# Kernel tuning notes

Hardware: AMD Instinct MI355X
Metric: run time of the kernel (lower is better)

The kernel has to match this reference:

```python
import jax, jax.numpy as jnp
import numpy as np
from jax import lax

B, T, D, H, L = 16, 1500, 512, 512, 2
LN_EPS = 1e-5


def _layernorm(v, w, b):
    m = jnp.mean(v, axis=-1, keepdims=True)
    var = jnp.mean(jnp.square(v - m), axis=-1, keepdims=True)
    return (v - m) * lax.rsqrt(var + LN_EPS) * w + b


def setup_inputs() -> dict:
    key = jax.random.key(0)
    k_x, k_wi, k_wh = jax.random.split(key, 3)
    x = jax.random.normal(k_x, (B, T, D), dtype=jnp.float32)
    # i2h / h2h weights: [L, 3H, in_dim] (input_size == hidden_size so stackable)
    Wi = jax.random.normal(k_wi, (L, 3 * H, D), dtype=jnp.float32) * 0.04
    Wh = jax.random.normal(k_wh, (L, 3 * H, H), dtype=jnp.float32) * 0.04
    # LayerNorm affine params for (r, z, n) per layer
    ln_w = jnp.ones((L, 3, H), dtype=jnp.float32)
    ln_b = jnp.zeros((L, 3, H), dtype=jnp.float32)
    return {"x": x, "Wi": Wi, "Wh": Wh, "ln_w": ln_w, "ln_b": ln_b}


def reference(x, Wi, Wh, ln_w, ln_b):
    n_layers = Wi.shape[0]
    hidden = Wh.shape[-1]
    batch = x.shape[0]

    def step(h_states, x_t):
        # h_states: [L, B, H]; x_t: [B, D]
        inp = x_t
        new_hs = []
        for l in range(n_layers):
            h = h_states[l]
            x_gates = inp @ Wi[l].T        # [B, 3H]
            h_gates = h @ Wh[l].T          # [B, 3H]
            x_r, x_z, x_n = jnp.split(x_gates, 3, axis=1)
            h_r, h_z, h_n = jnp.split(h_gates, 3, axis=1)
            r = jax.nn.sigmoid(_layernorm(x_r + h_r, ln_w[l, 0], ln_b[l, 0]))
            z = jax.nn.sigmoid(_layernorm(x_z + h_z, ln_w[l, 1], ln_b[l, 1]))
            n = jnp.tanh(_layernorm(x_n + r * h_n, ln_w[l, 2], ln_b[l, 2]))
            h_new = (1 - z) * n + z * h
            if l > 0:  # residual (Identity proj since in_dim == hidden)
                h_new = h_new + inp
            new_hs.append(h_new)
            inp = h_new  # dropout is identity in eval mode
        return jnp.stack(new_hs), new_hs[-1]

    h0 = jnp.zeros((n_layers, batch, hidden), dtype=x.dtype)
    xs = jnp.swapaxes(x, 0, 1)  # [T, B, D]
    _, outs = lax.scan(step, h0, xs)
    return jnp.swapaxes(outs, 0, 1)  # [B, T, H]
```

## Files before the change

### kernel.cpp

```cpp
#include <hip/hip_runtime.h>

typedef unsigned long long u64;
typedef unsigned int u32;
typedef unsigned short u16;
typedef _Float16 f16;
typedef _Float16 h2v __attribute__((ext_vector_type(2)));

#define BB 16
#define TT 1500
#define NG3 1536
#define GM (BB * TT)
#define GK 512
#define LNEPS 1e-5f
#define NWG 48
#define FL 64
#define H0D 8
#define H1D 4
#define HROWU 256
#define GROW 768

__device__ __forceinline__ float sigmoidf_(float x) { return 1.f / (1.f + __expf(-x)); }
__device__ __forceinline__ float tanhf_(float x) {
  x = fminf(15.f, fmaxf(-15.f, x));
  float e = __expf(2.f * x);
  return (e - 1.f) / (e + 1.f);
}
__device__ __forceinline__ float red16_(float v) {
  v += __shfl_xor(v, 1, 64); v += __shfl_xor(v, 2, 64);
  v += __shfl_xor(v, 4, 64); v += __shfl_xor(v, 8, 64);
  return v;
}
__device__ __forceinline__ float red64_(float v) {
  v = red16_(v);
  v += __shfl_xor(v, 16, 64); v += __shfl_xor(v, 32, 64);
  return v;
}
__device__ __forceinline__ u32 pkh2(float a, float b) {
  u16 sa = __builtin_bit_cast(u16, (f16)a);
  u16 sb = __builtin_bit_cast(u16, (f16)b);
  return (u32)sa | ((u32)sb << 16);
}
__device__ __forceinline__ float f16lo(u32 p) { u16 s = (u16)p; return (float)__builtin_bit_cast(f16, s); }
__device__ __forceinline__ float f16hi(u32 p) { u16 s = (u16)(p >> 16); return (float)__builtin_bit_cast(f16, s); }
__device__ __forceinline__ h2v bch2(u32 u) { return __builtin_bit_cast(h2v, u); }
__device__ __forceinline__ float dot2f(h2v a, h2v b, float c) {
#if __has_builtin(__builtin_amdgcn_fdot2)
  return __builtin_amdgcn_fdot2(a, b, c, false);
#else
  return fmaf((float)a.y, (float)b.y, fmaf((float)a.x, (float)b.x, c));
#endif
}
__device__ __forceinline__ int physp(int c) { return c ^ ((c >> 2) & 7); }

__device__ __forceinline__ u64 ldA(const u64* p) {
  return __hip_atomic_load(p, __ATOMIC_RELAXED, __HIP_MEMORY_SCOPE_AGENT);
}
__device__ __forceinline__ u32 ldA32(const u32* p) {
  return __hip_atomic_load(p, __ATOMIC_RELAXED, __HIP_MEMORY_SCOPE_AGENT);
}
__device__ __forceinline__ void stA32(u32* p, u32 v) {
  __hip_atomic_store(p, v, __ATOMIC_RELAXED, __HIP_MEMORY_SCOPE_AGENT);
}

__global__ __launch_bounds__(256) void gemm_nt(const float* __restrict__ A,
                                               const float* __restrict__ W,
                                               float* __restrict__ C) {
  __shared__ __align__(16) float As[32][68];
  __shared__ __align__(16) float Ws[32][68];
  const int m0 = blockIdx.x * 64;
  const int n0 = blockIdx.y * 64;
  const int tid = threadIdx.x;
  const int tm = tid & 15, tn = tid >> 4;
  float acc[4][4] = {};
  for (int k0 = 0; k0 < GK; k0 += 32) {
#pragma unroll
    for (int u = 0; u < 2; ++u) {
      int idx = tid + u * 256;
      int r = idx >> 3;
      int kq = (idx & 7) * 4;
      float4 a = *reinterpret_cast<const float4*>(&A[(size_t)(m0 + r) * GK + k0 + kq]);
      As[kq + 0][r] = a.x; As[kq + 1][r] = a.y; As[kq + 2][r] = a.z; As[kq + 3][r] = a.w;
      float4 w = *reinterpret_cast<const float4*>(&W[(size_t)(n0 + r) * GK + k0 + kq]);
      Ws[kq + 0][r] = w.x; Ws[kq + 1][r] = w.y; Ws[kq + 2][r] = w.z; Ws[kq + 3][r] = w.w;
    }
    __syncthreads();
#pragma unroll
    for (int kk = 0; kk < 32; ++kk) {
      float a[4], w[4];
      *reinterpret_cast<float4*>(a) = *reinterpret_cast<const float4*>(&As[kk][tm * 4]);
      *reinterpret_cast<float4*>(w) = *reinterpret_cast<const float4*>(&Ws[kk][tn * 4]);
#pragma unroll
      for (int i = 0; i < 4; ++i)
#pragma unroll
        for (int q = 0; q < 4; ++q)
          acc[i][q] = fmaf(a[i], w[q], acc[i][q]);
    }
    __syncthreads();
  }
#pragma unroll
  for (int i = 0; i < 4; ++i) {
    float4 v = make_float4(acc[i][0], acc[i][1], acc[i][2], acc[i][3]);
    *reinterpret_cast<float4*>(&C[(size_t)(m0 + tm * 4 + i) * NG3 + n0 + tn * 4]) = v;
  }
}

__global__ __launch_bounds__(256, 1) void gru_fused(
    const float* __restrict__ Wh0, const float* __restrict__ Wi1,
    const float* __restrict__ Wh1, const float* __restrict__ X0,
    const float* __restrict__ lnw, const float* __restrict__ lnb,
    float* __restrict__ out, u32* __restrict__ G0, u32* __restrict__ G1h,
    u32* __restrict__ G1x, u32* __restrict__ Hb0, u32* __restrict__ Hb1,
    u32* __restrict__ flags) {
  u32* flag0  = flags;
  u32* flag1h = flags + 48 * FL;
  u32* flag1x = flags + 96 * FL;
  u32* h0f    = flags + 144 * FL;
  u32* h1f    = flags + 160 * FL;

  __shared__ __align__(16) u16 shA[BB][544];
  __shared__ __align__(16) float red4[4][4];

  const int tid = threadIdx.x, wg = blockIdx.x;
  const int lane = tid & 63, wave = tid >> 6;
  const int ks = lane & 15, cq = lane >> 4;
  const int role = wg / NWG;
  const int wgl = wg - role * NWG;
  const int pairIdx = wgl * 16 + wave * 4 + cq;
  const int col0 = pairIdx * 2;
  const int rr = tid >> 4, q16 = tid & 15;

  const float* Wsel = (role == 0) ? Wh0 : (role == 1) ? Wh1 : Wi1;
  u32 wp[2][16];
#pragma unroll
  for (int c = 0; c < 2; ++c) {
    const float* Wp = Wsel + (size_t)(col0 + c) * 512 + ks * 32;
#pragma unroll
    for (int i = 0; i < 16; ++i) wp[c][i] = pkh2(Wp[2 * i], Wp[2 * i + 1]);
  }
  const bool own = (role <= 1) && (wgl < 16);
  const int b_own = wgl;
  const float* lnwL = lnw + (role == 1 ? NG3 : 0);
  const float* lnbL = lnb + (role == 1 ? NG3 : 0);
  float lwv[6], lbv[6];
  if (own) {
#pragma unroll
    for (int g = 0; g < 3; ++g)
#pragma unroll
      for (int c = 0; c < 2; ++c) {
        lwv[g * 2 + c] = lnwL[g * 512 + 2 * tid + c];
        lbv[g * 2 + c] = lnbL[g * 512 + 2 * tid + c];
      }
  }
  u32* Gst = (role == 0) ? G0 : (role == 1) ? G1h : G1x;
  u32* myflag = (role == 0) ? flag0 : (role == 1) ? flag1h : flag1x;

  for (int idx = tid; idx < BB * 544; idx += 256) (&shA[0][0])[idx] = 0;
  __syncthreads();

  for (int t = 0; t < TT; ++t) {
    const u32 want = (u32)(t + 1);

    if (role == 2) {
      if (tid < 16)
        while (ldA32(&h0f[(size_t)tid * FL]) < want) __builtin_amdgcn_s_sleep(1);
      __syncthreads();
      const u32* Hsrc = Hb0 + (size_t)(t & (H0D - 1)) * (BB * HROWU);
      const u64* src = (const u64*)(Hsrc + (size_t)rr * HROWU) + q16 * 8;
      u32 pl[16];
#pragma unroll
      for (int m = 0; m < 8; ++m) {
        u64 w = ldA(src + m);
        pl[2 * m] = (u32)w; pl[2 * m + 1] = (u32)(w >> 32);
      }
#pragma unroll
      for (int w = 0; w < 4; ++w)
        *reinterpret_cast<uint4*>(&shA[rr][physp(q16 * 4 + w) * 8]) =
            make_uint4(pl[4 * w], pl[4 * w + 1], pl[4 * w + 2], pl[4 * w + 3]);
      __syncthreads();
    } else if (t > 0) {
      u32* hf = (role == 0) ? h0f : h1f;
      if (tid < 16)
        while (ldA32(&hf[(size_t)tid * FL]) < (u32)t) __builtin_amdgcn_s_sleep(1);
      __syncthreads();
      const u32* Hsrc = (role == 0)
          ? Hb0 + (size_t)((t - 1) & (H0D - 1)) * (BB * HROWU)
          : Hb1 + (size_t)((t - 1) & (H1D - 1)) * (BB * HROWU);
      const u64* src = (const u64*)(Hsrc + (size_t)rr * HROWU) + q16 * 8;
      u32 pl[16];
#pragma unroll
      for (int m = 0; m < 8; ++m) {
        u64 w = ldA(src + m);
        pl[2 * m] = (u32)w; pl[2 * m + 1] = (u32)(w >> 32);
      }
#pragma unroll
      for (int w = 0; w < 4; ++w)
        *reinterpret_cast<uint4*>(&shA[rr][physp(q16 * 4 + w) * 8]) =
            make_uint4(pl[4 * w], pl[4 * w + 1], pl[4 * w + 2], pl[4 * w + 3]);
      __syncthreads();
    }

    float g0 = 0.f, g1 = 0.f;
#pragma unroll 4
    for (int b = 0; b < 16; ++b) {
      float p0 = 0.f, p1 = 0.f;
#pragma unroll
      for (int j = 0; j < 4; ++j) {
        const int idx = ((ks * 4 + j) ^ (ks & 7)) * 8;
        uint4 ua = *reinterpret_cast<const uint4*>(&shA[b][idx]);
        p0 = dot2f(bch2(ua.x), bch2(wp[0][j * 4 + 0]), p0);
        p0 = dot2f(bch2(ua.y), bch2(wp[0][j * 4 + 1]), p0);
        p0 = dot2f(bch2(ua.z), bch2(wp[0][j * 4 + 2]), p0);
        p0 = dot2f(bch2(ua.w), bch2(wp[0][j * 4 + 3]), p0);
        p1 = dot2f(bch2(ua.x), bch2(wp[1][j * 4 + 0]), p1);
        p1 = dot2f(bch2(ua.y), bch2(wp[1][j * 4 + 1]), p1);
        p1 = dot2f(bch2(ua.z), bch2(wp[1][j * 4 + 2]), p1);
        p1 = dot2f(bch2(ua.w), bch2(wp[1][j * 4 + 3]), p1);
      }
      p0 = red16_(p0); p1 = red16_(p1);
      if (ks == b) { g0 = p0; g1 = p1; }
    }
    if (role == 2 && t >= 2) {
      const u32 w2 = (u32)(t - 1);
      while (ldA32(&h1f[(size_t)(tid & 15) * FL]) < w2) __builtin_amdgcn_s_sleep(1);
    }
    stA32(&Gst[(size_t)(t & 1) * (BB * GROW) + (size_t)ks * GROW + pairIdx], pkh2(g0, g1));
    asm volatile("s_waitcnt vmcnt(0)" ::: "memory");
    __syncthreads();
    if (tid == 0) stA32(&myflag[(size_t)wgl * FL], want);

    if (own) {
      if (role == 0) {
        if (lane < 48)
          while (ldA32(&flag0[(size_t)lane * FL]) < want) __builtin_amdgcn_s_sleep(1);
      } else {
        if (lane < 48) {
          while (ldA32(&flag1h[(size_t)lane * FL]) < want) __builtin_amdgcn_s_sleep(1);
          while (ldA32(&flag1x[(size_t)lane * FL]) < want) __builtin_amdgcn_s_sleep(1);
        }
      }
      const size_t gbase = (size_t)(t & 1) * (BB * GROW) + (size_t)b_own * GROW + tid;
      float gr0, gr1, gz0, gz1, hn0, hn1, xn0, xn1;
      {
        const u32* Gr = (role == 0) ? G0 : G1h;
        u32 pr = ldA32(&Gr[gbase]);
        u32 pz = ldA32(&Gr[gbase + 256]);
        u32 pn = ldA32(&Gr[gbase + 512]);
        gr0 = f16lo(pr); gr1 = f16hi(pr);
        gz0 = f16lo(pz); gz1 = f16hi(pz);
        hn0 = f16lo(pn); hn1 = f16hi(pn);
      }
      if (role == 1) {
        u32 qr = ldA32(&G1x[gbase]);
        u32 qz = ldA32(&G1x[gbase + 256]);
        u32 qx = ldA32(&G1x[gbase + 512]);
        gr0 += f16lo(qr); gr1 += f16hi(qr);
        gz0 += f16lo(qz); gz1 += f16hi(qz);
        xn0 = f16lo(qx); xn1 = f16hi(qx);
      } else {
        const float* Xr = X0 + ((size_t)b_own * TT + t) * NG3 + 2 * tid;
        float2 xr = *reinterpret_cast<const float2*>(Xr);
        float2 xz = *reinterpret_cast<const float2*>(Xr + 512);
        float2 xl = *reinterpret_cast<const float2*>(Xr + 1024);
        gr0 += xr.x; gr1 += xr.y;
        gz0 += xz.x; gz1 += xz.y;
        xn0 = xl.x; xn1 = xl.y;
      }
      float sr = red64_(gr0 + gr1), sr2 = red64_(gr0 * gr0 + gr1 * gr1);
      float sz = red64_(gz0 + gz1), sz2 = red64_(gz0 * gz0 + gz1 * gz1);
      if (lane == 0) {
        red4[wave][0] = sr; red4[wave][1] = sr2;
        red4[wave][2] = sz; red4[wave][3] = sz2;
      }
      __syncthreads();
      float tsr = 0, tsr2 = 0, tsz = 0, tsz2 = 0;
#pragma unroll
      for (int w = 0; w < 4; ++w) {
        tsr += red4[w][0]; tsr2 += red4[w][1];
        tsz += red4[w][2]; tsz2 += red4[w][3];
      }
      const float mr = tsr * (1.f / 512.f);
      const float rsr = rsqrtf(tsr2 * (1.f / 512.f) - mr * mr + LNEPS);
      const float mz = tsz * (1.f / 512.f);
      const float rsz = rsqrtf(tsz2 * (1.f / 512.f) - mz * mz + LNEPS);
      const float rv0 = sigmoidf_((gr0 - mr) * rsr * lwv[0] + lbv[0]);
      const float rv1 = sigmoidf_((gr1 - mr) * rsr * lwv[1] + lbv[1]);
      const float zv0 = sigmoidf_((gz0 - mz) * rsz * lwv[2] + lbv[2]);
      const float zv1 = sigmoidf_((gz1 - mz) * rsz * lwv[3] + lbv[3]);
      const float np0 = xn0 + rv0 * hn0;
      const float np1 = xn1 + rv1 * hn1;
      float sn = red64_(np0 + np1), sn2 = red64_(np0 * np0 + np1 * np1);
      __syncthreads();
      if (lane == 0) { red4[wave][0] = sn; red4[wave][1] = sn2; }
      __syncthreads();
      float tn = red4[0][0] + red4[1][0] + red4[2][0] + red4[3][0];
      float tn2 = red4[0][1] + red4[1][1] + red4[2][1] + red4[3][1];
      const float mn = tn * (1.f / 512.f);
      const float rsn = rsqrtf(tn2 * (1.f / 512.f) - mn * mn + LNEPS);
      u32 hp = *reinterpret_cast<const u32*>(&shA[b_own][physp(tid >> 2) * 8 + 2 * (tid & 3)]);
      const float n0 = tanhf_((np0 - mn) * rsn * lwv[4] + lbv[4]);
      const float n1 = tanhf_((np1 - mn) * rsn * lwv[5] + lbv[5]);
      float hv0 = (1.f - zv0) * n0 + zv0 * f16lo(hp);
      float hv1 = (1.f - zv1) * n1 + zv1 * f16hi(hp);
      if (role == 1) {
        while (ldA32(&h0f[(size_t)b_own * FL]) < want) __builtin_amdgcn_s_sleep(1);
        u32 r0 = ldA32(&Hb0[(size_t)(t & (H0D - 1)) * (BB * HROWU) + (size_t)b_own * HROWU + tid]);
        hv0 += f16lo(r0); hv1 += f16hi(r0);
        *reinterpret_cast<float2*>(&out[((size_t)b_own * TT + t) * 512 + 2 * tid]) =
            make_float2(hv0, hv1);
      }
      if (role == 0 && t >= H0D) {
        const u32 w2 = (u32)(t - (H0D - 1));
        if (lane < 48)
          while (ldA32(&flag1x[(size_t)lane * FL]) < w2) __builtin_amdgcn_s_sleep(1);
        if (lane < 16)
          while (ldA32(&h1f[(size_t)lane * FL]) < w2) __builtin_amdgcn_s_sleep(1);
      }
      if (role == 1 && t >= H1D) {
        const u32 w2 = (u32)(t - 2);
        if (lane < 48)
          while (ldA32(&flag1h[(size_t)lane * FL]) < w2) __builtin_amdgcn_s_sleep(1);
      }
      u32* Hw = (role == 0)
          ? Hb0 + (size_t)(t & (H0D - 1)) * (BB * HROWU) + (size_t)b_own * HROWU
          : Hb1 + (size_t)(t & (H1D - 1)) * (BB * HROWU) + (size_t)b_own * HROWU;
      stA32(&Hw[tid], pkh2(hv0, hv1));
      asm volatile("s_waitcnt vmcnt(0)" ::: "memory");
      __syncthreads();
      if (tid == 0) stA32(&((role == 0) ? h0f : h1f)[(size_t)b_own * FL], want);
    }
  }
}

extern "C" void kernel_launch(void* const* d_in, const int* in_sizes, int n_in,
                              void* d_out, int out_size, void* d_ws, size_t ws_size,
                              hipStream_t stream) {
  (void)in_sizes; (void)n_in; (void)out_size; (void)ws_size;
  const float* x   = (const float*)d_in[0];
  const float* Wi  = (const float*)d_in[1];
  const float* Wh  = (const float*)d_in[2];
  const float* lnw = (const float*)d_in[3];
  const float* lnb = (const float*)d_in[4];
  float* out = (float*)d_out;

  float* X0 = (float*)d_ws;
  u32* G0   = (u32*)(X0 + (size_t)GM * NG3);
  u32* G1h  = G0 + 2 * BB * GROW;
  u32* G1x  = G1h + 2 * BB * GROW;
  u32* Hb0  = G1x + 2 * BB * GROW;
  u32* Hb1  = Hb0 + H0D * BB * HROWU;
  u32* flags = Hb1 + H1D * BB * HROWU;

  size_t clear_bytes = (size_t)(3 * 2 * BB * GROW + H0D * BB * HROWU +
                                H1D * BB * HROWU + 176 * FL) * 4;
  hipMemsetAsync(G0, 0, clear_bytes, stream);

  dim3 ggrid(GM / 64, NG3 / 64);
  gemm_nt<<<ggrid, 256, 0, stream>>>(x, Wi, X0);
  gru_fused<<<3 * NWG, 256, 0, stream>>>(
      Wh, Wi + (size_t)NG3 * 512, Wh + (size_t)NG3 * 512, X0, lnw, lnb, out,
      G0, G1h, G1x, Hb0, Hb1, flags);
}
```

Before: 17.28 ms.

## Replace flag-based inter-workgroup sync with step-tagged 64-bit data words

Each 32-bit packed f16 value in the gate and hidden-state exchange buffers now travels inside a 64-bit word with the timestep in the upper half. Consumers spin on the data itself until every tag matches, so producers no longer need the vmcnt wait, block barrier and separate flag store. This removes a round trip and two barriers per step on the serial recurrence path. It also drops one __syncthreads in the layernorm reduction by using separate red4 slots. The cost is double the exchange traffic and wider polling loads. Correctness depends on 64-bit atomic stores being single-copy atomic.

```diff
diff --git a/kernel.cpp b/kernel.cpp
--- a/kernel.cpp
+++ b/kernel.cpp
@@ -13,10 +13,9 @@
 #define GK 512
 #define LNEPS 1e-5f
 #define NWG 48
-#define FL 64
 #define H0D 8
 #define H1D 4
-#define HROWU 256
+#define HROW 256
 #define GROW 768
 
 __device__ __forceinline__ float sigmoidf_(float x) { return 1.f / (1.f + __expf(-x)); }
@@ -55,11 +54,11 @@
 __device__ __forceinline__ u64 ldA(const u64* p) {
   return __hip_atomic_load(p, __ATOMIC_RELAXED, __HIP_MEMORY_SCOPE_AGENT);
 }
-__device__ __forceinline__ u32 ldA32(const u32* p) {
-  return __hip_atomic_load(p, __ATOMIC_RELAXED, __HIP_MEMORY_SCOPE_AGENT);
-}
-__device__ __forceinline__ void stA32(u32* p, u32 v) {
+__device__ __forceinline__ void stA8(u64* p, u64 v) {
   __hip_atomic_store(p, v, __ATOMIC_RELAXED, __HIP_MEMORY_SCOPE_AGENT);
+}
+__device__ __forceinline__ u64 mkw(u32 tag, float a, float b) {
+  return ((u64)tag << 32) | (u64)pkh2(a, b);
 }
 
 __global__ __launch_bounds__(256) void gemm_nt(const float* __restrict__ A,
@@ -108,17 +107,10 @@
     const float* __restrict__ Wh0, const float* __restrict__ Wi1,
     const float* __restrict__ Wh1, const float* __restrict__ X0,
     const float* __restrict__ lnw, const float* __restrict__ lnb,
-    float* __restrict__ out, u32* __restrict__ G0, u32* __restrict__ G1h,
-    u32* __restrict__ G1x, u32* __restrict__ Hb0, u32* __restrict__ Hb1,
-    u32* __restrict__ flags) {
-  u32* flag0  = flags;
-  u32* flag1h = flags + 48 * FL;
-  u32* flag1x = flags + 96 * FL;
-  u32* h0f    = flags + 144 * FL;
-  u32* h1f    = flags + 160 * FL;
-
+    float* __restrict__ out, u64* __restrict__ G0, u64* __restrict__ G1h,
+    u64* __restrict__ G1x, u64* __restrict__ Hb0, u64* __restrict__ Hb1) {
   __shared__ __align__(16) u16 shA[BB][544];
-  __shared__ __align__(16) float red4[4][4];
+  __shared__ __align__(16) float red4[4][6];
 
   const int tid = threadIdx.x, wg = blockIdx.x;
   const int lane = tid & 63, wave = tid >> 6;
@@ -151,8 +143,7 @@
         lbv[g * 2 + c] = lnbL[g * 512 + 2 * tid + c];
       }
   }
-  u32* Gst = (role == 0) ? G0 : (role == 1) ? G1h : G1x;
-  u32* myflag = (role == 0) ? flag0 : (role == 1) ? flag1h : flag1x;
+  u64* Gst = (role == 0) ? G0 : (role == 1) ? G1h : G1x;
 
   for (int idx = tid; idx < BB * 544; idx += 256) (&shA[0][0])[idx] = 0;
   __syncthreads();
@@ -160,43 +151,43 @@
   for (int t = 0; t < TT; ++t) {
     const u32 want = (u32)(t + 1);
 
-    if (role == 2) {
-      if (tid < 16)
-        while (ldA32(&h0f[(size_t)tid * FL]) < want) __builtin_amdgcn_s_sleep(1);
-      __syncthreads();
-      const u32* Hsrc = Hb0 + (size_t)(t & (H0D - 1)) * (BB * HROWU);
-      const u64* src = (const u64*)(Hsrc + (size_t)rr * HROWU) + q16 * 8;
-      u32 pl[16];
-#pragma unroll
-      for (int m = 0; m < 8; ++m) {
-        u64 w = ldA(src + m);
-        pl[2 * m] = (u32)w; pl[2 * m + 1] = (u32)(w >> 32);
-      }
-#pragma unroll
-      for (int w = 0; w < 4; ++w)
-        *reinterpret_cast<uint4*>(&shA[rr][physp(q16 * 4 + w) * 8]) =
-            make_uint4(pl[4 * w], pl[4 * w + 1], pl[4 * w + 2], pl[4 * w + 3]);
-      __syncthreads();
-    } else if (t > 0) {
-      u32* hf = (role == 0) ? h0f : h1f;
-      if (tid < 16)
-        while (ldA32(&hf[(size_t)tid * FL]) < (u32)t) __builtin_amdgcn_s_sleep(1);
-      __syncthreads();
-      const u32* Hsrc = (role == 0)
-          ? Hb0 + (size_t)((t - 1) & (H0D - 1)) * (BB * HROWU)
-          : Hb1 + (size_t)((t - 1) & (H1D - 1)) * (BB * HROWU);
-      const u64* src = (const u64*)(Hsrc + (size_t)rr * HROWU) + q16 * 8;
-      u32 pl[16];
-#pragma unroll
-      for (int m = 0; m < 8; ++m) {
-        u64 w = ldA(src + m);
-        pl[2 * m] = (u32)w; pl[2 * m + 1] = (u32)(w >> 32);
-      }
-#pragma unroll
-      for (int w = 0; w < 4; ++w)
-        *reinterpret_cast<uint4*>(&shA[rr][physp(q16 * 4 + w) * 8]) =
-            make_uint4(pl[4 * w], pl[4 * w + 1], pl[4 * w + 2], pl[4 * w + 3]);
-      __syncthreads();
+    {
+      const u64* src = nullptr;
+      u32 wantH = 0;
+      if (role == 2) {
+        src = Hb0 + (size_t)(t & (H0D - 1)) * (BB * HROW);
+        wantH = want;
+      } else if (t > 0) {
+        src = (role == 0)
+            ? Hb0 + (size_t)((t - 1) & (H0D - 1)) * (BB * HROW)
+            : Hb1 + (size_t)((t - 1) & (H1D - 1)) * (BB * HROW);
+        wantH = (u32)t;
+      }
+      if (src) {
+        const u64* p = src + (size_t)rr * HROW + q16 * 16;
+        u32 pl[16];
+        for (;;) {
+          u32 bad = 0;
+          u64 w[16];
+#pragma unroll
+          for (int m = 0; m < 16; ++m) {
+            w[m] = ldA(p + m);
+            bad |= (u32)(w[m] >> 32) ^ wantH;
+          }
+          if (!bad) {
+#pragma unroll
+            for (int m = 0; m < 16; ++m) pl[m] = (u32)w[m];
+            break;
+          }
+          __builtin_amdgcn_s_sleep(1);
+        }
+        __syncthreads();
+#pragma unroll
+        for (int w2 = 0; w2 < 4; ++w2)
+          *reinterpret_cast<uint4*>(&shA[rr][physp(q16 * 4 + w2) * 8]) =
+              make_uint4(pl[4 * w2], pl[4 * w2 + 1], pl[4 * w2 + 2], pl[4 * w2 + 3]);
+        __syncthreads();
+      }
     }
 
     float g0 = 0.f, g1 = 0.f;
@@ -221,49 +212,57 @@
     }
     if (role == 2 && t >= 2) {
       const u32 w2 = (u32)(t - 1);
-      while (ldA32(&h1f[(size_t)(tid & 15) * FL]) < w2) __builtin_amdgcn_s_sleep(1);
-    }
-    stA32(&Gst[(size_t)(t & 1) * (BB * GROW) + (size_t)ks * GROW + pairIdx], pkh2(g0, g1));
-    asm volatile("s_waitcnt vmcnt(0)" ::: "memory");
-    __syncthreads();
-    if (tid == 0) stA32(&myflag[(size_t)wgl * FL], want);
+      const u64* hb = Hb1 + (size_t)((t - 2) & (H1D - 1)) * (BB * HROW) +
+                      (size_t)(tid & 15) * HROW;
+      while ((u32)(ldA(hb) >> 32) < w2) __builtin_amdgcn_s_sleep(1);
+      asm volatile("" ::: "memory");
+    }
+    stA8(&Gst[(size_t)(t & 1) * (BB * GROW) + (size_t)ks * GROW + pairIdx],
+         ((u64)want << 32) | (u64)pkh2(g0, g1));
 
     if (own) {
+      float xr0 = 0, xr1 = 0, xz0 = 0, xz1 = 0, xpn0 = 0, xpn1 = 0;
       if (role == 0) {
-        if (lane < 48)
-          while (ldA32(&flag0[(size_t)lane * FL]) < want) __builtin_amdgcn_s_sleep(1);
-      } else {
-        if (lane < 48) {
-          while (ldA32(&flag1h[(size_t)lane * FL]) < want) __builtin_amdgcn_s_sleep(1);
-          while (ldA32(&flag1x[(size_t)lane * FL]) < want) __builtin_amdgcn_s_sleep(1);
+        const float* Xr = X0 + ((size_t)b_own * TT + t) * NG3 + 2 * tid;
+        float2 a = *reinterpret_cast<const float2*>(Xr);
+        float2 b = *reinterpret_cast<const float2*>(Xr + 512);
+        float2 c = *reinterpret_cast<const float2*>(Xr + 1024);
+        xr0 = a.x; xr1 = a.y; xz0 = b.x; xz1 = b.y; xpn0 = c.x; xpn1 = c.y;
+      }
+      const u64* Gr = ((role == 0) ? G0 : G1h) +
+                      (size_t)(t & 1) * (BB * GROW) + (size_t)b_own * GROW;
+      const u64* Gx = G1x + (size_t)(t & 1) * (BB * GROW) + (size_t)b_own * GROW;
+      float gr0, gr1, gz0, gz1, hn0, hn1, xg0, xg1;
+      for (;;) {
+        u32 bad = 0;
+        u64 pr = ldA(&Gr[tid]);
+        u64 pz = ldA(&Gr[tid + 256]);
+        u64 pn = ldA(&Gr[tid + 512]);
+        bad = ((u32)(pr >> 32) ^ want) | ((u32)(pz >> 32) ^ want) |
+              ((u32)(pn >> 32) ^ want);
+        u64 qr = 0, qz = 0, qx = 0;
+        if (role == 1) {
+          qr = ldA(&Gx[tid]);
+          qz = ldA(&Gx[tid + 256]);
+          qx = ldA(&Gx[tid + 512]);
+          bad |= ((u32)(qr >> 32) ^ want) | ((u32)(qz >> 32) ^ want) |
+                 ((u32)(qx >> 32) ^ want);
         }
-      }
-      const size_t gbase = (size_t)(t & 1) * (BB * GROW) + (size_t)b_own * GROW + tid;
-      float gr0, gr1, gz0, gz1, hn0, hn1, xn0, xn1;
-      {
-        const u32* Gr = (role == 0) ? G0 : G1h;
-        u32 pr = ldA32(&Gr[gbase]);
-        u32 pz = ldA32(&Gr[gbase + 256]);
-        u32 pn = ldA32(&Gr[gbase + 512]);
-        gr0 = f16lo(pr); gr1 = f16hi(pr);
-        gz0 = f16lo(pz); gz1 = f16hi(pz);
-        hn0 = f16lo(pn); hn1 = f16hi(pn);
-      }
-      if (role == 1) {
-        u32 qr = ldA32(&G1x[gbase]);
-        u32 qz = ldA32(&G1x[gbase + 256]);
-        u32 qx = ldA32(&G1x[gbase + 512]);
-        gr0 += f16lo(qr); gr1 += f16hi(qr);
-        gz0 += f16lo(qz); gz1 += f16hi(qz);
-        xn0 = f16lo(qx); xn1 = f16hi(qx);
-      } else {
-        const float* Xr = X0 + ((size_t)b_own * TT + t) * NG3 + 2 * tid;
-        float2 xr = *reinterpret_cast<const float2*>(Xr);
-        float2 xz = *reinterpret_cast<const float2*>(Xr + 512);
-        float2 xl = *reinterpret_cast<const float2*>(Xr + 1024);
-        gr0 += xr.x; gr1 += xr.y;
-        gz0 += xz.x; gz1 += xz.y;
-        xn0 = xl.x; xn1 = xl.y;
+        if (!bad) {
+          gr0 = f16lo((u32)pr); gr1 = f16hi((u32)pr);
+          gz0 = f16lo((u32)pz); gz1 = f16hi((u32)pz);
+          hn0 = f16lo((u32)pn); hn1 = f16hi((u32)pn);
+          if (role == 1) {
+            gr0 += f16lo((u32)qr); gr1 += f16hi((u32)qr);
+            gz0 += f16lo((u32)qz); gz1 += f16hi((u32)qz);
+            xg0 = f16lo((u32)qx); xg1 = f16hi((u32)qx);
+          } else {
+            gr0 += xr0; gr1 += xr1; gz0 += xz0; gz1 += xz1;
+            xg0 = xpn0; xg1 = xpn1;
+          }
+          break;
+        }
+        __builtin_amdgcn_s_sleep(1);
       }
       float sr = red64_(gr0 + gr1), sr2 = red64_(gr0 * gr0 + gr1 * gr1);
       float sz = red64_(gz0 + gz1), sz2 = red64_(gz0 * gz0 + gz1 * gz1);
@@ -286,47 +285,42 @@
       const float rv1 = sigmoidf_((gr1 - mr) * rsr * lwv[1] + lbv[1]);
       const float zv0 = sigmoidf_((gz0 - mz) * rsz * lwv[2] + lbv[2]);
       const float zv1 = sigmoidf_((gz1 - mz) * rsz * lwv[3] + lbv[3]);
-      const float np0 = xn0 + rv0 * hn0;
-      const float np1 = xn1 + rv1 * hn1;
+      const float np0 = xg0 + rv0 * hn0;
+      const float np1 = xg1 + rv1 * hn1;
       float sn = red64_(np0 + np1), sn2 = red64_(np0 * np0 + np1 * np1);
+      if (lane == 0) { red4[wave][4] = sn; red4[wave][5] = sn2; }
       __syncthreads();
-      if (lane == 0) { red4[wave][0] = sn; red4[wave][1] = sn2; }
-      __syncthreads();
-      float tn = red4[0][0] + red4[1][0] + red4[2][0] + red4[3][0];
-      float tn2 = red4[0][1] + red4[1][1] + red4[2][1] + red4[3][1];
+      float tn = red4[0][4] + red4[1][4] + red4[2][4] + red4[3][4];
+      float tn2 = red4[0][5] + red4[1][5] + red4[2][5] + red4[3][5];
       const float mn = tn * (1.f / 512.f);
       const float rsn = rsqrtf(tn2 * (1.f / 512.f) - mn * mn + LNEPS);
-      u32 hp = *reinterpret_cast<const u32*>(&shA[b_own][physp(tid >> 2) * 8 + 2 * (tid & 3)]);
+      u32 hp = *reinterpret_cast<const u32*>(
+          &shA[b_own][physp(tid >> 2) * 8 + 2 * (tid & 3)]);
       const float n0 = tanhf_((np0 - mn) * rsn * lwv[4] + lbv[4]);
       const float n1 = tanhf_((np1 - mn) * rsn * lwv[5] + lbv[5]);
       float hv0 = (1.f - zv0) * n0 + zv0 * f16lo(hp);
       float hv1 = (1.f - zv1) * n1 + zv1 * f16hi(hp);
       if (role == 1) {
-        while (ldA32(&h0f[(size_t)b_own * FL]) < want) __builtin_amdgcn_s_sleep(1);
-        u32 r0 = ldA32(&Hb0[(size_t)(t & (H0D - 1)) * (BB * HROWU) + (size_t)b_own * HROWU + tid]);
-        hv0 += f16lo(r0); hv1 += f16hi(r0);
+        const u64* Hr = Hb0 + (size_t)(t & (H0D - 1)) * (BB * HROW) +
+                        (size_t)b_own * HROW + tid;
+        u64 w;
+        while ((u32)((w = ldA(Hr)) >> 32) != want) __builtin_amdgcn_s_sleep(1);
+        hv0 += f16lo((u32)w); hv1 += f16hi((u32)w);
         *reinterpret_cast<float2*>(&out[((size_t)b_own * TT + t) * 512 + 2 * tid]) =
             make_float2(hv0, hv1);
       }
       if (role == 0 && t >= H0D) {
         const u32 w2 = (u32)(t - (H0D - 1));
-        if (lane < 48)
-          while (ldA32(&flag1x[(size_t)lane * FL]) < w2) __builtin_amdgcn_s_sleep(1);
-        if (lane < 16)
-          while (ldA32(&h1f[(size_t)lane * FL]) < w2) __builtin_amdgcn_s_sleep(1);
-      }
-      if (role == 1 && t >= H1D) {
-        const u32 w2 = (u32)(t - 2);
-        if (lane < 48)
-          while (ldA32(&flag1h[(size_t)lane * FL]) < w2) __builtin_amdgcn_s_sleep(1);
-      }
-      u32* Hw = (role == 0)
-          ? Hb0 + (size_t)(t & (H0D - 1)) * (BB * HROWU) + (size_t)b_own * HROWU
-          : Hb1 + (size_t)(t & (H1D - 1)) * (BB * HROWU) + (size_t)b_own * HROWU;
-      stA32(&Hw[tid], pkh2(hv0, hv1));
-      asm volatile("s_waitcnt vmcnt(0)" ::: "memory");
-      __syncthreads();
-      if (tid == 0) stA32(&((role == 0) ? h0f : h1f)[(size_t)b_own * FL], want);
+        const u64* hb = Hb1 + (size_t)((t - H0D) & (H1D - 1)) * (BB * HROW) +
+                        (size_t)(tid & 15) * HROW;
+        while ((u32)(ldA(hb) >> 32) < w2) __builtin_amdgcn_s_sleep(1);
+        asm volatile("" ::: "memory");
+      }
+      u64* Hw = ((role == 0)
+                     ? Hb0 + (size_t)(t & (H0D - 1)) * (BB * HROW)
+                     : Hb1 + (size_t)(t & (H1D - 1)) * (BB * HROW)) +
+                (size_t)b_own * HROW;
+      stA8(&Hw[tid], ((u64)want << 32) | (u64)pkh2(hv0, hv1));
     }
   }
 }
@@ -343,20 +337,19 @@
   float* out = (float*)d_out;
 
   float* X0 = (float*)d_ws;
-  u32* G0   = (u32*)(X0 + (size_t)GM * NG3);
-  u32* G1h  = G0 + 2 * BB * GROW;
-  u32* G1x  = G1h + 2 * BB * GROW;
-  u32* Hb0  = G1x + 2 * BB * GROW;
-  u32* Hb1  = Hb0 + H0D * BB * HROWU;
-  u32* flags = Hb1 + H1D * BB * HROWU;
-
-  size_t clear_bytes = (size_t)(3 * 2 * BB * GROW + H0D * BB * HROWU +
-                                H1D * BB * HROWU + 176 * FL) * 4;
+  u64* G0   = (u64*)(X0 + (size_t)GM * NG3);
+  u64* G1h  = G0 + 2 * BB * GROW;
+  u64* G1x  = G1h + 2 * BB * GROW;
+  u64* Hb0  = G1x + 2 * BB * GROW;
+  u64* Hb1  = Hb0 + (size_t)H0D * BB * HROW;
+
+  size_t clear_bytes = (size_t)(3 * 2 * BB * GROW + H0D * BB * HROW +
+                                H1D * BB * HROW) * 8;
   hipMemsetAsync(G0, 0, clear_bytes, stream);
 
   dim3 ggrid(GM / 64, NG3 / 64);
   gemm_nt<<<ggrid, 256, 0, stream>>>(x, Wi, X0);
   gru_fused<<<3 * NWG, 256, 0, stream>>>(
       Wh, Wi + (size_t)NG3 * 512, Wh + (size_t)NG3 * 512, X0, lnw, lnb, out,
-      G0, G1h, G1x, Hb0, Hb1, flags);
-}
+      G0, G1h, G1x, Hb0, Hb1);
+}
```

Result: slower. 21.25 ms (+22.9%).
